# Kernel tuning notes

Measured on AMD Instinct MI355X. Metric: run time of the kernel, lower is better.

The kernel has to match this reference:

```python
import jax, jax.numpy as jnp
import numpy as np

HIDDEN = 768
META = 25
ED_COUNT = 300
B, N_MENT, N_PAIRS = 2, 2000, 40000


def setup_inputs() -> dict:
    key = jax.random.key(0)
    ks = jax.random.split(key, 8)
    mention_reprs = jax.random.normal(ks[0], (B, N_MENT, HIDDEN), dtype=jnp.float32)
    coref_mention_pairs = jax.random.randint(ks[1], (B, N_PAIRS, 2), 0, N_MENT)
    coref_eds = jax.random.randint(ks[2], (B, N_PAIRS), 0, ED_COUNT)
    in_dim = HIDDEN * 2 + META
    # nn.Linear default init scale ~ 1/sqrt(fan_in); exact init is irrelevant for correctness
    W1 = jax.random.normal(ks[3], (in_dim, HIDDEN), dtype=jnp.float32) / np.sqrt(in_dim)
    b1 = jnp.zeros((HIDDEN,), dtype=jnp.float32)
    W2 = jax.random.normal(ks[4], (HIDDEN, 1), dtype=jnp.float32) / np.sqrt(HIDDEN)
    b2 = jnp.zeros((1,), dtype=jnp.float32)
    ed_table = jax.random.normal(ks[5], (ED_COUNT, META), dtype=jnp.float32)
    return {
        "mention_reprs": mention_reprs,
        "coref_mention_pairs": coref_mention_pairs,
        "coref_eds": coref_eds,
        "ed_table": ed_table,
        "W1": W1,
        "b1": b1,
        "W2": W2,
        "b2": b2,
    }


def reference(mention_reprs, coref_mention_pairs, coref_eds, ed_table, W1, b1, W2, b2):
    b = mention_reprs.shape[0]
    # batch_index gather: [B, P, 2, H]
    bidx = jnp.arange(b)[:, None, None]
    pairs = mention_reprs[bidx, coref_mention_pairs]
    # flatten pair dim -> [B, P, 2H]
    pair_repr = pairs.reshape(b, pairs.shape[1], -1)
    eds = ed_table[coref_eds]  # [B, P, META]
    coref_repr = jnp.concatenate([pair_repr, eds], axis=2)  # [B, P, 2H+META]
    h = jax.nn.relu(coref_repr @ W1 + b1)  # dropout = identity in eval
    logits = (h @ W2 + b2).squeeze(-1)  # [B, P]
    return logits
```

## Files before the change

kernel.cpp:

```cpp
#include <hip/hip_runtime.h>
#include <stdint.h>

#define HIDDEN 768
#define META 25
#define EDC 300
#define BB 2
#define NMENT 2000
#define NPAIRS 40000
#define M_ROWS (BB * NMENT)
#define M_PAD 4096
#define N_OUT 1536
#define TOTAL_PAIRS (BB * NPAIRS)
#define BK 64

typedef __bf16 bf16x8 __attribute__((ext_vector_type(8)));
typedef float f32x4 __attribute__((ext_vector_type(4)));

static __device__ __forceinline__ float bf2f(unsigned short u) {
    union { unsigned int u; float f; } v; v.u = ((unsigned int)u) << 16; return v.f;
}
static __device__ __forceinline__ float2 bf2x(unsigned int u) {
    union { unsigned int x; float f; } lo, hi;
    lo.x = u << 16; hi.x = u & 0xffff0000u;
    float2 r; r.x = lo.f; r.y = hi.f; return r;
}
static __device__ __forceinline__ unsigned short f2bf(float f) {
    union { float f; unsigned int u; } v; v.f = f;
    unsigned int u = v.u;
    unsigned int r = (u + 0x7FFFu + ((u >> 16) & 1u)) >> 16;
    return (unsigned short)r;
}

#define GLOAD_LDS16(g, l)                                                            \
    __builtin_amdgcn_global_load_lds((const __attribute__((address_space(1))) void*)(g), \
                                     (__attribute__((address_space(3))) void*)(l), 16, 0, 0)

#define NB_CONVM 3072
#define NB_CONVW 576
#define NB_PREP  900
#define NB_W2    3

__global__ __launch_bounds__(256) void k_prep_all(
        const float* __restrict__ M, unsigned short* __restrict__ Mb,
        const float* __restrict__ W1, unsigned short* __restrict__ Wt,
        const float* __restrict__ ed_table, const float* __restrict__ b1,
        unsigned short* __restrict__ Epp,
        const float* __restrict__ W2, unsigned short* __restrict__ W2b) {
    const int blk = blockIdx.x;
    const int t = threadIdx.x;
    if (blk < NB_CONVM) {
        int idx = (blk * 256 + t) * 4;
        int row = idx / HIDDEN;
        ushort4 o;
        if (row < M_ROWS) {
            const float4 v = *(const float4*)(M + idx);
            o.x = f2bf(v.x); o.y = f2bf(v.y); o.z = f2bf(v.z); o.w = f2bf(v.w);
        } else {
            o.x = 0; o.y = 0; o.z = 0; o.w = 0;
        }
        *(ushort4*)(Mb + idx) = o;
    } else if (blk < NB_CONVM + NB_CONVW) {
        __shared__ float tile[32][68];
        int id = blk - NB_CONVM;
        int nt = id % 24, kt = id / 24;
        int n0 = nt * 64, k0 = kt * 32;
        int tk = t >> 4, tn = (t & 15) * 4;
        int srcRowOff = (n0 < HIDDEN) ? 0 : HIDDEN;
        int srcColBase = (n0 < HIDDEN) ? n0 : (n0 - HIDDEN);
        {
            const float4 v0 = *(const float4*)(W1 + (size_t)(k0 + tk + srcRowOff) * HIDDEN + srcColBase + tn);
            tile[tk][tn] = v0.x; tile[tk][tn + 1] = v0.y; tile[tk][tn + 2] = v0.z; tile[tk][tn + 3] = v0.w;
            const float4 v1 = *(const float4*)(W1 + (size_t)(k0 + tk + 16 + srcRowOff) * HIDDEN + srcColBase + tn);
            tile[tk + 16][tn] = v1.x; tile[tk + 16][tn + 1] = v1.y; tile[tk + 16][tn + 2] = v1.z; tile[tk + 16][tn + 3] = v1.w;
        }
        __syncthreads();
        int wn = t >> 2, wk = (t & 3) * 8;
        unsigned int p0 = (unsigned int)f2bf(tile[wk + 0][wn]) | ((unsigned int)f2bf(tile[wk + 1][wn]) << 16);
        unsigned int p1 = (unsigned int)f2bf(tile[wk + 2][wn]) | ((unsigned int)f2bf(tile[wk + 3][wn]) << 16);
        unsigned int p2 = (unsigned int)f2bf(tile[wk + 4][wn]) | ((unsigned int)f2bf(tile[wk + 5][wn]) << 16);
        unsigned int p3 = (unsigned int)f2bf(tile[wk + 6][wn]) | ((unsigned int)f2bf(tile[wk + 7][wn]) << 16);
        uint4 pk; pk.x = p0; pk.y = p1; pk.z = p2; pk.w = p3;
        *(uint4*)(Wt + (size_t)(n0 + wn) * HIDDEN + k0 + wk) = pk;
    } else if (blk < NB_CONVM + NB_CONVW + NB_PREP) {
        int id = (blk - NB_CONVM - NB_CONVW) * 256 + t;
        int e = id / HIDDEN, n = id - e * HIDDEN;
        float acc = b1[n];
#pragma unroll
        for (int k = 0; k < META; k++)
            acc += ed_table[e * META + k] * W1[(size_t)(2 * HIDDEN + k) * HIDDEN + n];
        Epp[id] = f2bf(acc);
    } else {
        int id = (blk - NB_CONVM - NB_CONVW - NB_PREP) * 256 + t;
        if (id < HIDDEN) W2b[id] = f2bf(W2[id]);
    }
}

__global__ __launch_bounds__(256) void k_gemm(const unsigned short* __restrict__ Mb,
                                              const unsigned short* __restrict__ Wt,
                                              unsigned short* __restrict__ AW) {
    __shared__ unsigned short As[128 * BK];
    __shared__ unsigned short Bs[64 * BK];
    const int m0 = blockIdx.x * 128;
    const int n0 = blockIdx.y * 64;
    const int t = threadIdx.x, w = t >> 6, lane = t & 63;
    const int wm = (w & 1) * 64, wn = (w >> 1) * 32;
    const int q = lane >> 4, r = lane & 15;
    const int lrow = lane >> 3;
    const int lcol = ((((lane & 7) - lrow) & 7)) * 8;
    const unsigned short* gA = Mb + (size_t)(m0 + w * 32 + lrow) * HIDDEN + lcol;
    const unsigned short* gB = Wt + (size_t)(n0 + w * 16 + lrow) * HIDDEN + lcol;
    unsigned short* lA = As + (w * 32) * BK;
    unsigned short* lB = Bs + (w * 16) * BK;
    f32x4 acc[4][2] = {};
    for (int k0 = 0; k0 < HIDDEN; k0 += BK) {
        GLOAD_LDS16(gA + k0, lA);
        GLOAD_LDS16(gA + k0 + 8 * HIDDEN,  lA + 8 * BK);
        GLOAD_LDS16(gA + k0 + 16 * HIDDEN, lA + 16 * BK);
        GLOAD_LDS16(gA + k0 + 24 * HIDDEN, lA + 24 * BK);
        GLOAD_LDS16(gB + k0, lB);
        GLOAD_LDS16(gB + k0 + 8 * HIDDEN,  lB + 8 * BK);
        __syncthreads();
        bf16x8 af[4][2], bfr[2][2];
        const int rs = r & 7;
#pragma unroll
        for (int i = 0; i < 4; i++)
#pragma unroll
            for (int s = 0; s < 2; s++)
                af[i][s] = *(const bf16x8*)&As[(wm + i * 16 + r) * BK + 8 * ((q + 4 * s + rs) & 7)];
#pragma unroll
        for (int j = 0; j < 2; j++)
#pragma unroll
            for (int s = 0; s < 2; s++)
                bfr[j][s] = *(const bf16x8*)&Bs[(wn + j * 16 + r) * BK + 8 * ((q + 4 * s + rs) & 7)];
#pragma unroll
        for (int i = 0; i < 4; i++)
#pragma unroll
            for (int j = 0; j < 2; j++) {
                acc[i][j] = __builtin_amdgcn_mfma_f32_16x16x32_bf16(af[i][0], bfr[j][0], acc[i][j], 0, 0, 0);
                acc[i][j] = __builtin_amdgcn_mfma_f32_16x16x32_bf16(af[i][1], bfr[j][1], acc[i][j], 0, 0, 0);
            }
        __syncthreads();
    }
    const int colb = n0 + wn + (lane & 15);
    const int rowb = m0 + wm + (lane >> 4) * 4;
#pragma unroll
    for (int i = 0; i < 4; i++)
#pragma unroll
        for (int j = 0; j < 2; j++) {
            unsigned short* dst = AW + (size_t)(rowb + i * 16) * N_OUT + colb + j * 16;
#pragma unroll
            for (int reg = 0; reg < 4; reg++)
                dst[(size_t)reg * N_OUT] = f2bf(acc[i][j][reg]);
        }
}

__global__ __launch_bounds__(256, 6) void k_pair(const unsigned short* __restrict__ AW,
                                                 const unsigned short* __restrict__ Epp,
                                                 const unsigned short* __restrict__ W2b,
                                                 const float* __restrict__ b2,
                                                 const int* __restrict__ pairs,
                                                 const int* __restrict__ eds,
                                                 float* __restrict__ out) {
    const int wid = blockIdx.x * 4 + (threadIdx.x >> 6);
    const int lane = threadIdx.x & 63;
    const int hl = lane & 31;
    const bool lo = lane < 32;
    const int p0 = wid * 2;
    const size_t base = (p0 >= NPAIRS) ? (size_t)NMENT : 0;

    const int4 pr = *(const int4*)(pairs + (size_t)p0 * 2);
    const int2 e2 = *(const int2*)(eds + p0);
    const int m1 = lo ? pr.x : pr.z;
    const int m2 = lo ? pr.y : pr.w;
    const int ed = lo ? e2.x : e2.y;

    const int n = hl * 24;
    const unsigned short* A1 = AW + (base + m1) * N_OUT + n;
    const unsigned short* A2 = AW + (base + m2) * N_OUT + HIDDEN + n;
    const unsigned short* EP = Epp + (size_t)ed * HIDDEN + n;
    const unsigned short* WW = W2b + n;

    uint4 a0 = *(const uint4*)(A1);
    uint4 a1v = *(const uint4*)(A1 + 8);
    uint4 a2v = *(const uint4*)(A1 + 16);
    uint4 c0 = *(const uint4*)(A2);
    uint4 c1 = *(const uint4*)(A2 + 8);
    uint4 c2 = *(const uint4*)(A2 + 16);
    uint4 e0 = *(const uint4*)(EP);
    uint4 e1 = *(const uint4*)(EP + 8);
    uint4 e2v = *(const uint4*)(EP + 16);
    uint4 w0 = *(const uint4*)(WW);
    uint4 w1 = *(const uint4*)(WW + 8);
    uint4 w2v = *(const uint4*)(WW + 16);

    float acc = 0.f;
#define ACC2(ua, ub, ue, uw)                                                   \
    {                                                                          \
        float2 fa = bf2x(ua), fb = bf2x(ub), fe = bf2x(ue), fw = bf2x(uw);     \
        float h0 = fmaxf(fa.x + fb.x + fe.x, 0.f);                             \
        float h1 = fmaxf(fa.y + fb.y + fe.y, 0.f);                             \
        acc += h0 * fw.x + h1 * fw.y;                                          \
    }
    ACC2(a0.x, c0.x, e0.x, w0.x); ACC2(a0.y, c0.y, e0.y, w0.y);
    ACC2(a0.z, c0.z, e0.z, w0.z); ACC2(a0.w, c0.w, e0.w, w0.w);
    ACC2(a1v.x, c1.x, e1.x, w1.x); ACC2(a1v.y, c1.y, e1.y, w1.y);
    ACC2(a1v.z, c1.z, e1.z, w1.z); ACC2(a1v.w, c1.w, e1.w, w1.w);
    ACC2(a2v.x, c2.x, e2v.x, w2v.x); ACC2(a2v.y, c2.y, e2v.y, w2v.y);
    ACC2(a2v.z, c2.z, e2v.z, w2v.z); ACC2(a2v.w, c2.w, e2v.w, w2v.w);
#undef ACC2

#pragma unroll
    for (int o = 16; o > 0; o >>= 1)
        acc += __shfl_xor(acc, o, 64);

    if (hl == 0)
        out[p0 + (lane >> 5)] = acc + b2[0];
}

extern "C" void kernel_launch(void* const* d_in, const int* in_sizes, int n_in,
                              void* d_out, int out_size, void* d_ws, size_t ws_size,
                              hipStream_t stream) {
    const float* mention  = (const float*)d_in[0];
    const int*   pairs    = (const int*)d_in[1];
    const int*   eds      = (const int*)d_in[2];
    const float* ed_table = (const float*)d_in[3];
    const float* W1       = (const float*)d_in[4];
    const float* b1       = (const float*)d_in[5];
    const float* W2       = (const float*)d_in[6];
    const float* b2       = (const float*)d_in[7];
    float* out = (float*)d_out;

    char* ws = (char*)d_ws;
    unsigned short* Mb  = (unsigned short*)(ws);
    unsigned short* Wt  = (unsigned short*)(ws + 6291456);
    unsigned short* AW  = (unsigned short*)(ws + 8650752);
    unsigned short* Epp = (unsigned short*)(ws + 21233664);
    unsigned short* W2b = (unsigned short*)(ws + 21694464);

    k_prep_all<<<dim3(NB_CONVM + NB_CONVW + NB_PREP + NB_W2), dim3(256), 0, stream>>>(
        mention, Mb, W1, Wt, ed_table, b1, Epp, W2, W2b);
    k_gemm<<<dim3(M_PAD / 128, N_OUT / 64), dim3(256), 0, stream>>>(Mb, Wt, AW);
    k_pair<<<dim3(TOTAL_PAIRS / 8), dim3(256), 0, stream>>>(AW, Epp, W2b, b2, pairs, eds, out);
}
```

Baseline: 135.3 us.

## Split pair kernel's hidden dimension across four blocks and combine with atomics

The pair-scoring kernel now splits the 768-wide hidden reduction into four 192-column chunks, each handled by a separate block, and combines the partial dot products with atomicAdd into an output that the prep kernel zeroes first. Block indices are interleaved so consecutive blocks share the same pairs and hit the same rows in cache. This aims for more parallelism and smaller per-thread loads, at the cost of four times the pair/index reads, 12-byte loads, and atomic traffic on the output.

```diff
diff --git a/kernel.cpp b/kernel.cpp
--- a/kernel.cpp
+++ b/kernel.cpp
@@ -39,13 +39,15 @@
 #define NB_CONVW 576
 #define NB_PREP  900
 #define NB_W2    3
+#define NB_ZOUT  79
 
 __global__ __launch_bounds__(256) void k_prep_all(
         const float* __restrict__ M, unsigned short* __restrict__ Mb,
         const float* __restrict__ W1, unsigned short* __restrict__ Wt,
         const float* __restrict__ ed_table, const float* __restrict__ b1,
         unsigned short* __restrict__ Epp,
-        const float* __restrict__ W2, unsigned short* __restrict__ W2b) {
+        const float* __restrict__ W2, unsigned short* __restrict__ W2b,
+        float* __restrict__ out) {
     const int blk = blockIdx.x;
     const int t = threadIdx.x;
     if (blk < NB_CONVM) {
@@ -89,9 +91,15 @@
         for (int k = 0; k < META; k++)
             acc += ed_table[e * META + k] * W1[(size_t)(2 * HIDDEN + k) * HIDDEN + n];
         Epp[id] = f2bf(acc);
-    } else {
+    } else if (blk < NB_CONVM + NB_CONVW + NB_PREP + NB_W2) {
         int id = (blk - NB_CONVM - NB_CONVW - NB_PREP) * 256 + t;
         if (id < HIDDEN) W2b[id] = f2bf(W2[id]);
+    } else {
+        int i4 = (blk - (NB_CONVM + NB_CONVW + NB_PREP + NB_W2)) * 256 + t;
+        if (i4 * 4 < TOTAL_PAIRS) {
+            float4 z; z.x = 0.f; z.y = 0.f; z.z = 0.f; z.w = 0.f;
+            *(float4*)(out + i4 * 4) = z;
+        }
     }
 }
 
@@ -154,67 +162,63 @@
         }
 }
 
-__global__ __launch_bounds__(256, 6) void k_pair(const unsigned short* __restrict__ AW,
-                                                 const unsigned short* __restrict__ Epp,
-                                                 const unsigned short* __restrict__ W2b,
-                                                 const float* __restrict__ b2,
-                                                 const int* __restrict__ pairs,
-                                                 const int* __restrict__ eds,
-                                                 float* __restrict__ out) {
-    const int wid = blockIdx.x * 4 + (threadIdx.x >> 6);
+__global__ __launch_bounds__(256) void k_pair(const unsigned short* __restrict__ AW,
+                                              const unsigned short* __restrict__ Epp,
+                                              const unsigned short* __restrict__ W2b,
+                                              const float* __restrict__ b2,
+                                              const int* __restrict__ pairs,
+                                              const int* __restrict__ eds,
+                                              float* __restrict__ out) {
+    const int bi = blockIdx.x;
+    const int slot = bi & 7;
+    const int idx  = bi >> 3;
+    const int batch = slot >> 2;
+    const int c     = slot & 3;
+    const int w = threadIdx.x >> 6;
     const int lane = threadIdx.x & 63;
     const int hl = lane & 31;
     const bool lo = lane < 32;
-    const int p0 = wid * 2;
-    const size_t base = (p0 >= NPAIRS) ? (size_t)NMENT : 0;
-
-    const int4 pr = *(const int4*)(pairs + (size_t)p0 * 2);
-    const int2 e2 = *(const int2*)(eds + p0);
+    const int pidx = batch * NPAIRS + (idx * 4 + w) * 2;
+    const size_t base = (size_t)batch * NMENT;
+
+    const int4 pr = *(const int4*)(pairs + (size_t)pidx * 2);
+    const int2 e2 = *(const int2*)(eds + pidx);
     const int m1 = lo ? pr.x : pr.z;
     const int m2 = lo ? pr.y : pr.w;
     const int ed = lo ? e2.x : e2.y;
 
-    const int n = hl * 24;
-    const unsigned short* A1 = AW + (base + m1) * N_OUT + n;
-    const unsigned short* A2 = AW + (base + m2) * N_OUT + HIDDEN + n;
-    const unsigned short* EP = Epp + (size_t)ed * HIDDEN + n;
-    const unsigned short* WW = W2b + n;
-
-    uint4 a0 = *(const uint4*)(A1);
-    uint4 a1v = *(const uint4*)(A1 + 8);
-    uint4 a2v = *(const uint4*)(A1 + 16);
-    uint4 c0 = *(const uint4*)(A2);
-    uint4 c1 = *(const uint4*)(A2 + 8);
-    uint4 c2 = *(const uint4*)(A2 + 16);
-    uint4 e0 = *(const uint4*)(EP);
-    uint4 e1 = *(const uint4*)(EP + 8);
-    uint4 e2v = *(const uint4*)(EP + 16);
-    uint4 w0 = *(const uint4*)(WW);
-    uint4 w1 = *(const uint4*)(WW + 8);
-    uint4 w2v = *(const uint4*)(WW + 16);
+    const int nb = c * 192 + hl * 6;
+    const unsigned short* A1 = AW + (base + m1) * N_OUT + nb;
+    const unsigned short* A2 = AW + (base + m2) * N_OUT + HIDDEN + nb;
+    const unsigned short* EP = Epp + (size_t)ed * HIDDEN + nb;
+    const unsigned short* WW = W2b + nb;
+
+    const uint3 ua = *(const uint3*)A1;
+    const uint3 ub = *(const uint3*)A2;
+    const uint3 ue = *(const uint3*)EP;
+    const uint3 uw = *(const uint3*)WW;
 
     float acc = 0.f;
-#define ACC2(ua, ub, ue, uw)                                                   \
+#define ACC2(ua_, ub_, ue_, uw_)                                               \
     {                                                                          \
-        float2 fa = bf2x(ua), fb = bf2x(ub), fe = bf2x(ue), fw = bf2x(uw);     \
+        float2 fa = bf2x(ua_), fb = bf2x(ub_), fe = bf2x(ue_), fw = bf2x(uw_); \
         float h0 = fmaxf(fa.x + fb.x + fe.x, 0.f);                             \
         float h1 = fmaxf(fa.y + fb.y + fe.y, 0.f);                             \
         acc += h0 * fw.x + h1 * fw.y;                                          \
     }
-    ACC2(a0.x, c0.x, e0.x, w0.x); ACC2(a0.y, c0.y, e0.y, w0.y);
-    ACC2(a0.z, c0.z, e0.z, w0.z); ACC2(a0.w, c0.w, e0.w, w0.w);
-    ACC2(a1v.x, c1.x, e1.x, w1.x); ACC2(a1v.y, c1.y, e1.y, w1.y);
-    ACC2(a1v.z, c1.z, e1.z, w1.z); ACC2(a1v.w, c1.w, e1.w, w1.w);
-    ACC2(a2v.x, c2.x, e2v.x, w2v.x); ACC2(a2v.y, c2.y, e2v.y, w2v.y);
-    ACC2(a2v.z, c2.z, e2v.z, w2v.z); ACC2(a2v.w, c2.w, e2v.w, w2v.w);
+    ACC2(ua.x, ub.x, ue.x, uw.x);
+    ACC2(ua.y, ub.y, ue.y, uw.y);
+    ACC2(ua.z, ub.z, ue.z, uw.z);
 #undef ACC2
 
 #pragma unroll
     for (int o = 16; o > 0; o >>= 1)
         acc += __shfl_xor(acc, o, 64);
 
-    if (hl == 0)
-        out[p0 + (lane >> 5)] = acc + b2[0];
+    if (hl == 0) {
+        float v = acc + ((c == 0) ? b2[0] : 0.f);
+        atomicAdd(out + pidx + (lane >> 5), v);
+    }
 }
 
 extern "C" void kernel_launch(void* const* d_in, const int* in_sizes, int n_in,
@@ -237,8 +241,8 @@
     unsigned short* Epp = (unsigned short*)(ws + 21233664);
     unsigned short* W2b = (unsigned short*)(ws + 21694464);
 
-    k_prep_all<<<dim3(NB_CONVM + NB_CONVW + NB_PREP + NB_W2), dim3(256), 0, stream>>>(
-        mention, Mb, W1, Wt, ed_table, b1, Epp, W2, W2b);
+    k_prep_all<<<dim3(NB_CONVM + NB_CONVW + NB_PREP + NB_W2 + NB_ZOUT), dim3(256), 0, stream>>>(
+        mention, Mb, W1, Wt, ed_table, b1, Epp, W2, W2b, out);
     k_gemm<<<dim3(M_PAD / 128, N_OUT / 64), dim3(256), 0, stream>>>(Mb, Wt, AW);
-    k_pair<<<dim3(TOTAL_PAIRS / 8), dim3(256), 0, stream>>>(AW, Epp, W2b, b2, pairs, eds, out);
-}
+    k_pair<<<dim3(TOTAL_PAIRS / 2), dim3(256), 0, stream>>>(AW, Epp, W2b, b2, pairs, eds, out);
+}
```

Result: no change. 132.9 us (-1.8%).
